# Performance work log

Hardware: AMD Instinct MI355X
Metric: run time of the kernel (lower is better)

The kernel has to match this reference:

```python
import jax, jax.numpy as jnp
import numpy as np

B, T, SZ, H = 16, 512, 512, 8
HD = SZ // H
D0, STD, GAMMA = 6.3, 1.4, 2.0
MAX_RPE = 16

def _dwconv(x, w):
    # depthwise conv1d, kernel 5, pad 2, groups=C, no bias; x: [B,T,C], w: [C,1,5]
    y = jax.lax.conv_general_dilated(x.transpose(0, 2, 1), w, (1,), [(2, 2)],
        dimension_numbers=('NCH', 'OIH', 'NCH'), feature_group_count=x.shape[-1])
    return y.transpose(0, 2, 1)

def _forward(mask, key, value, query, Wq, bq, Wk, bk, Wv, bv, Wcq, Wck, Wcv, Wgq, bgq, Wgk, bgk, Wgv, bgv, WmD, bmD, rpe_table, Wo, bo):
    q = query @ Wq.T + bq
    k = key @ Wk.T + bk
    v = value @ Wv.T + bv
    xn = key  # x_norm := key in the original forward
    # gated depthwise-conv context injection (qkv_context=[1,1,1], fuse='gate')
    qc = _dwconv(xn, Wcq)
    g = jax.nn.sigmoid(jnp.concatenate([q, qc], -1) @ Wgq.T + bgq)
    q = (1 - g) * q + g * qc
    kc = _dwconv(xn, Wck)
    g = jax.nn.sigmoid(jnp.concatenate([k, kc], -1) @ Wgk.T + bgk)
    k = (1 - g) * k + g * kc
    vc = _dwconv(xn, Wcv)
    g = jax.nn.sigmoid(jnp.concatenate([v, vc], -1) @ Wgv.T + bgv)
    v = (1 - g) * v + g * vc
    # learned Gaussian width: mod_D='head_share', mod_src='Q'
    off = (q @ WmD.T + bmD)[..., 0]                       # [B,T]
    m_D = D0 + 2.0 * STD * jnp.tanh(off / GAMMA)          # [B,T]
    qh = q.reshape(B, T, H, HD).transpose(0, 2, 1, 3) / jnp.sqrt(jnp.float32(HD))
    kh = k.reshape(B, T, H, HD).transpose(0, 2, 1, 3)
    vh = v.reshape(B, T, H, HD).transpose(0, 2, 1, 3)
    scores = jnp.einsum('bhqd,bhkd->bhqk', qh, kh)        # [B,H,T,T]
    idx = jnp.arange(T)
    d_int = idx[:, None] - idx[None, :]                   # i - j
    rd = jnp.clip(-d_int, -MAX_RPE, MAX_RPE) + MAX_RPE    # rpe indices [T,T]
    rpe = rpe_table[rd]                                   # [T,T,2*HD]
    rpe_k, rpe_v = rpe[..., :HD], rpe[..., HD:]
    scores = scores + jnp.einsum('bhqd,qkd->bhqk', qh, rpe_k)
    dist = d_int.astype(jnp.float32)
    scores = scores - dist ** 2 / (m_D[:, None, :, None] ** 2 / 2.0)
    scores = jnp.where(mask[:, None, :, :], -jnp.inf, scores)
    attn = jax.nn.softmax(scores, axis=-1)                # dropout is identity at eval
    ctx = jnp.einsum('bhqk,bhkd->bhqd', attn, vh) + jnp.einsum('bhqk,qkd->bhqd', attn, rpe_v)
    out = ctx.transpose(0, 2, 1, 3).reshape(B, T, SZ) @ Wo.T + bo
    return out

def setup_inputs():
    rng = jax.random.key(0)
    ks = jax.random.split(rng, 20)
    s = 0.02
    lin = lambda k, o, i: jax.random.normal(k, (o, i), jnp.float32) * s
    lengths = jax.random.randint(ks[3], (B,), T // 2, T + 1)
    mask = (jnp.arange(T)[None, :] >= lengths[:, None])[:, None, :]  # [B,1,T], True = pad
    return {
        'key': jax.random.normal(ks[0], (B, T, SZ), jnp.float32),
        'value': jax.random.normal(ks[1], (B, T, SZ), jnp.float32),
        'query': jax.random.normal(ks[2], (B, T, SZ), jnp.float32),
        'mask': mask,
        'Wq': lin(ks[4], SZ, SZ), 'bq': jnp.zeros((SZ,), jnp.float32),
        'Wk': lin(ks[5], SZ, SZ), 'bk': jnp.zeros((SZ,), jnp.float32),
        'Wv': lin(ks[6], SZ, SZ), 'bv': jnp.zeros((SZ,), jnp.float32),
        'Wcq': jax.random.normal(ks[7], (SZ, 1, 5), jnp.float32) * s,
        'Wck': jax.random.normal(ks[8], (SZ, 1, 5), jnp.float32) * s,
        'Wcv': jax.random.normal(ks[9], (SZ, 1, 5), jnp.float32) * s,
        'Wgq': lin(ks[10], 1, 2 * SZ), 'bgq': jnp.zeros((1,), jnp.float32),
        'Wgk': lin(ks[11], 1, 2 * SZ), 'bgk': jnp.zeros((1,), jnp.float32),
        'Wgv': lin(ks[12], 1, 2 * SZ), 'bgv': jnp.zeros((1,), jnp.float32),
        'WmD': lin(ks[13], 1, SZ), 'bmD': jnp.zeros((1,), jnp.float32),
        'rpe_table': jax.random.normal(ks[14], (2 * MAX_RPE + 1, 2 * HD), jnp.float32) * s,
        'Wo': lin(ks[15], SZ, SZ), 'bo': jnp.zeros((SZ,), jnp.float32),
    }

def reference(key, value, query, mask, Wq, bq, Wk, bk, Wv, bv, Wcq, Wck, Wcv, Wgq, bgq, Wgk, bgk, Wgv, bgv, WmD, bmD, rpe_table, Wo, bo):
    return _forward(mask, key, value, query, Wq, bq, Wk, bk, Wv, bv, Wcq, Wck, Wcv, Wgq, bgq, Wgk, bgk, Wgv, bgv, WmD, bmD, rpe_table, Wo, bo)
```

## Files before the change

### kernel.cpp

```cpp
#include <hip/hip_runtime.h>
#include <math.h>

#define NB 16
#define NT 512
#define NSZ 512
#define NH 8
#define NHD 64
#define MAXR 16

#define C_D0 6.3f
#define C_STD 1.4f
#define C_GAMMA 2.0f

#define NEGINF (-1e30f)
#define LOG2E 1.4426950408889634f
#define C1F   0.18033688011112042f

typedef unsigned short u16;
typedef __attribute__((ext_vector_type(8))) short bf16x8;
typedef __attribute__((ext_vector_type(4))) float f32x4;
typedef __attribute__((ext_vector_type(8))) unsigned short u16x8;
typedef __attribute__((ext_vector_type(4))) unsigned short u16x4;

__device__ __forceinline__ u16 f2b(float f) {
    union { float f; unsigned int u; } c; c.f = f;
    unsigned int u = c.u + 0x7FFFu + ((c.u >> 16) & 1u);
    return (u16)(u >> 16);
}
__device__ __forceinline__ float b2f(u16 h) {
    union { unsigned int u; float f; } c; c.u = ((unsigned int)h) << 16;
    return c.f;
}

#if __has_builtin(__builtin_amdgcn_exp2f)
__device__ __forceinline__ float exp2_fast(float x) { return __builtin_amdgcn_exp2f(x); }
#else
__device__ __forceinline__ float exp2_fast(float x) { return exp2f(x); }
#endif

#define GL2LDS(gp, lp) __builtin_amdgcn_global_load_lds( \
    (const __attribute__((address_space(1))) void*)(gp), \
    (__attribute__((address_space(3))) void*)(lp), 16, 0, 0)

#define SWU(r, c) ((((r) * 8) + ((c) ^ ((r) & 7))) * 8)
#define SWU16(r, c) ((((r) * 16) + ((c) ^ ((r) & 7))) * 8)

__global__ __launch_bounds__(256) void cvt4_bf16(
    const float* __restrict__ s0, const float* __restrict__ s1,
    const float* __restrict__ s2, const float* __restrict__ s3,
    u16* __restrict__ d0, u16* __restrict__ d1,
    u16* __restrict__ d2, u16* __restrict__ d3, int n)
{
    const float* s; u16* d;
    switch (blockIdx.y) {
        case 0: s = s0; d = d0; break;
        case 1: s = s1; d = d1; break;
        case 2: s = s2; d = d2; break;
        default: s = s3; d = d3; break;
    }
    int i = (blockIdx.x * 256 + threadIdx.x) * 8;
    if (i >= n) return;
    float4 a = *(const float4*)&s[i];
    float4 b = *(const float4*)&s[i + 4];
    u16x8 v;
    v[0]=f2b(a.x); v[1]=f2b(a.y); v[2]=f2b(a.z); v[3]=f2b(a.w);
    v[4]=f2b(b.x); v[5]=f2b(b.y); v[6]=f2b(b.z); v[7]=f2b(b.w);
    *(u16x8*)&d[i] = v;
}

__global__ __launch_bounds__(256) void wprep(
    const float* __restrict__ Wcq, const float* __restrict__ Wck,
    const float* __restrict__ Wcv, float* __restrict__ WcT)
{
    const int z = blockIdx.y;
    const float* src = z == 0 ? Wcq : (z == 1 ? Wck : Wcv);
    int idx = blockIdx.x * 256 + threadIdx.x;
    if (idx >= 2560) return;
    int c = idx / 5, j = idx % 5;
    WcT[(size_t)z * 2560 + j * 512 + c] = src[idx];
}

__global__ __launch_bounds__(256) void gemm_qkv(
    const float* __restrict__ A0, const float* __restrict__ A1, const float* __restrict__ A2,
    const u16* __restrict__ Wc,
    const float* __restrict__ bq, const float* __restrict__ bk, const float* __restrict__ bv,
    u16* __restrict__ pkv)
{
    __shared__ u16 Al[2][64 * 32];
    __shared__ u16 Bl[2][256 * 32];
    const int z = blockIdx.z;
    const float* A = z == 0 ? A0 : (z == 1 ? A1 : A2);
    const u16* W = Wc + (size_t)z * NSZ * NSZ;
    const float* bias = z == 0 ? bq : (z == 1 ? bk : bv);
    const int tid = threadIdx.x;
    const int m0 = blockIdx.x * 64;
    const int n0 = blockIdx.y * 256;
    const int w = tid >> 6, lane = tid & 63;
    const int wm = (w >> 1) * 32, wn = (w & 1) * 128;
    const int fr = lane & 15, fk = lane >> 4;

    const int arow = tid >> 2, acb = tid & 3;

    f32x4 acc[2][8] = {};

    {
        const float* ga = &A[(size_t)(m0 + arow) * NSZ + acb * 8];
        float4 a0 = *(const float4*)ga, a1 = *(const float4*)(ga + 4);
        #pragma unroll
        for (int p = 0; p < 4; ++p) {
            int s = tid + p * 256;
            int row = s >> 2, cb = s & 3;
            GL2LDS(&W[(size_t)(n0 + row) * NSZ + cb * 8], &Bl[0][s * 8]);
        }
        u16x8 v;
        v[0]=f2b(a0.x); v[1]=f2b(a0.y); v[2]=f2b(a0.z); v[3]=f2b(a0.w);
        v[4]=f2b(a1.x); v[5]=f2b(a1.y); v[6]=f2b(a1.z); v[7]=f2b(a1.w);
        *(u16x8*)&Al[0][tid * 8] = v;
    }
    __syncthreads();

    for (int t = 0; t < 16; ++t) {
        const int cur = t & 1, nxt = cur ^ 1;
        float4 a0n, a1n;
        const bool pre = (t < 15);
        if (pre) {
            const int k0 = (t + 1) * 32;
            const float* ga = &A[(size_t)(m0 + arow) * NSZ + k0 + acb * 8];
            a0n = *(const float4*)ga;
            a1n = *(const float4*)(ga + 4);
            #pragma unroll
            for (int p = 0; p < 4; ++p) {
                int s = tid + p * 256;
                int row = s >> 2, cb = s & 3;
                GL2LDS(&W[(size_t)(n0 + row) * NSZ + k0 + cb * 8], &Bl[nxt][s * 8]);
            }
        }
        bf16x8 af[2], bfr[8];
        #pragma unroll
        for (int mf = 0; mf < 2; ++mf)
            af[mf] = *(const bf16x8*)&Al[cur][(wm + mf * 16 + fr) * 32 + fk * 8];
        #pragma unroll
        for (int nf = 0; nf < 8; ++nf)
            bfr[nf] = *(const bf16x8*)&Bl[cur][(wn + nf * 16 + fr) * 32 + fk * 8];
        #pragma unroll
        for (int mf = 0; mf < 2; ++mf)
            #pragma unroll
            for (int nf = 0; nf < 8; ++nf)
                acc[mf][nf] = __builtin_amdgcn_mfma_f32_16x16x32_bf16(
                    af[mf], bfr[nf], acc[mf][nf], 0, 0, 0);
        if (pre) {
            u16x8 v;
            v[0]=f2b(a0n.x); v[1]=f2b(a0n.y); v[2]=f2b(a0n.z); v[3]=f2b(a0n.w);
            v[4]=f2b(a1n.x); v[5]=f2b(a1n.y); v[6]=f2b(a1n.z); v[7]=f2b(a1n.w);
            *(u16x8*)&Al[nxt][tid * 8] = v;
        }
        __syncthreads();
    }
    #pragma unroll
    for (int mf = 0; mf < 2; ++mf) {
        #pragma unroll
        for (int nf = 0; nf < 8; ++nf) {
            int col = n0 + wn + nf * 16 + fr;
            float bvv = bias[col];
            #pragma unroll
            for (int r = 0; r < 4; ++r) {
                int rowg = m0 + wm + mf * 16 + fk * 4 + r;
                pkv[(size_t)rowg * 1536 + z * 512 + col] = f2b(acc[mf][nf][r] + bvv);
            }
        }
    }
}

__global__ __launch_bounds__(256) void gemm_out(
    const u16* __restrict__ A, const u16* __restrict__ W,
    const float* __restrict__ bias, float* __restrict__ Cout, int M, int N, int K)
{
    __shared__ u16 Al[2][64 * 32];
    __shared__ u16 Bl[2][128 * 32];
    const int tid = threadIdx.x;
    const int m0 = blockIdx.x * 64;
    const int n0 = blockIdx.y * 128;
    const int w = tid >> 6, lane = tid & 63;
    const int wm = (w >> 1) * 32, wn = (w & 1) * 64;
    const int fr = lane & 15, fk = lane >> 4;

    f32x4 acc[2][4] = {};

    {
        int row = tid >> 2, cb = tid & 3;
        GL2LDS(&A[(size_t)(m0 + row) * K + cb * 8], &Al[0][tid * 8]);
        #pragma unroll
        for (int p = 0; p < 2; ++p) {
            int s = tid + p * 256;
            int r2 = s >> 2, c2 = s & 3;
            GL2LDS(&W[(size_t)(n0 + r2) * K + c2 * 8], &Bl[0][s * 8]);
        }
    }
    __syncthreads();

    const int nsteps = K / 32;
    for (int t = 0; t < nsteps; ++t) {
        const int cur = t & 1, nxt = cur ^ 1;
        if (t + 1 < nsteps) {
            const int k0 = (t + 1) * 32;
            int row = tid >> 2, cb = tid & 3;
            GL2LDS(&A[(size_t)(m0 + row) * K + k0 + cb * 8], &Al[nxt][tid * 8]);
            #pragma unroll
            for (int p = 0; p < 2; ++p) {
                int s = tid + p * 256;
                int r2 = s >> 2, c2 = s & 3;
                GL2LDS(&W[(size_t)(n0 + r2) * K + k0 + c2 * 8], &Bl[nxt][s * 8]);
            }
        }
        bf16x8 af[2], bfr[4];
        #pragma unroll
        for (int mf = 0; mf < 2; ++mf)
            af[mf] = *(const bf16x8*)&Al[cur][(wm + mf * 16 + fr) * 32 + fk * 8];
        #pragma unroll
        for (int nf = 0; nf < 4; ++nf)
            bfr[nf] = *(const bf16x8*)&Bl[cur][(wn + nf * 16 + fr) * 32 + fk * 8];
        #pragma unroll
        for (int mf = 0; mf < 2; ++mf)
            #pragma unroll
            for (int nf = 0; nf < 4; ++nf)
                acc[mf][nf] = __builtin_amdgcn_mfma_f32_16x16x32_bf16(
                    af[mf], bfr[nf], acc[mf][nf], 0, 0, 0);
        __syncthreads();
    }
    #pragma unroll
    for (int mf = 0; mf < 2; ++mf) {
        #pragma unroll
        for (int nf = 0; nf < 4; ++nf) {
            int col = n0 + wn + nf * 16 + fr;
            float bv = bias[col];
            #pragma unroll
            for (int r = 0; r < 4; ++r) {
                int rowg = m0 + wm + mf * 16 + fk * 4 + r;
                Cout[(size_t)rowg * N + col] = acc[mf][nf][r] + bv;
            }
        }
    }
}

__global__ void conv_gate_all(
    const float* __restrict__ xn, u16* __restrict__ pkv,
    u16* __restrict__ vpT,
    const float* __restrict__ WcT,
    const float* __restrict__ Wgq, const float* __restrict__ bgq,
    const float* __restrict__ Wgk, const float* __restrict__ bgk,
    const float* __restrict__ Wgv, const float* __restrict__ bgv,
    const float* __restrict__ WmD, const float* __restrict__ bmD,
    float* __restrict__ mD)
{
    __shared__ u16 lt[4][512];
    const int w = threadIdx.x >> 6, lane = threadIdx.x & 63;
    const int bt = blockIdx.x * 4 + w;
    const int b = bt >> 9, tpos = bt & (NT - 1);
    const int c0 = lane * 8;

    float x[5][8];
    #pragma unroll
    for (int j = 0; j < 5; ++j) {
        int tt = tpos + j - 2;
        if (tt >= 0 && tt < NT) {
            const float4* xp = (const float4*)&xn[((size_t)(b*NT + tt))*NSZ + c0];
            float4 u0 = xp[0], u1 = xp[1];
            x[j][0]=u0.x; x[j][1]=u0.y; x[j][2]=u0.z; x[j][3]=u0.w;
            x[j][4]=u1.x; x[j][5]=u1.y; x[j][6]=u1.z; x[j][7]=u1.w;
        } else {
            #pragma unroll
            for (int i = 0; i < 8; ++i) x[j][i] = 0.f;
        }
    }
    float aq[8] = {}, ak[8] = {}, av[8] = {};
    #pragma unroll
    for (int j = 0; j < 5; ++j) {
        const float* wq = &WcT[j * 512 + c0];
        const float* wk = &WcT[2560 + j * 512 + c0];
        const float* wv = &WcT[5120 + j * 512 + c0];
        float4 q0 = *(const float4*)wq, q1 = *(const float4*)(wq + 4);
        float4 k0 = *(const float4*)wk, k1 = *(const float4*)(wk + 4);
        float4 v0 = *(const float4*)wv, v1 = *(const float4*)(wv + 4);
        float wq8[8] = {q0.x,q0.y,q0.z,q0.w,q1.x,q1.y,q1.z,q1.w};
        float wk8[8] = {k0.x,k0.y,k0.z,k0.w,k1.x,k1.y,k1.z,k1.w};
        float wv8[8] = {v0.x,v0.y,v0.z,v0.w,v1.x,v1.y,v1.z,v1.w};
        #pragma unroll
        for (int i = 0; i < 8; ++i) {
            aq[i] += x[j][i] * wq8[i];
            ak[i] += x[j][i] * wk8[i];
            av[i] += x[j][i] * wv8[i];
        }
    }
    const size_t rb = (size_t)bt * 1536;
    u16x8 q8 = *(const u16x8*)&pkv[rb + c0];
    u16x8 k8 = *(const u16x8*)&pkv[rb + 512 + c0];
    u16x8 v8 = *(const u16x8*)&pkv[rb + 1024 + c0];

    float gql[8], gqh[8], gkl[8], gkh[8], gvl[8], gvh[8];
    {
        float4 a0 = *(const float4*)&Wgq[c0],      a1 = *(const float4*)&Wgq[c0 + 4];
        float4 a2 = *(const float4*)&Wgq[512 + c0], a3 = *(const float4*)&Wgq[512 + c0 + 4];
        gql[0]=a0.x;gql[1]=a0.y;gql[2]=a0.z;gql[3]=a0.w;gql[4]=a1.x;gql[5]=a1.y;gql[6]=a1.z;gql[7]=a1.w;
        gqh[0]=a2.x;gqh[1]=a2.y;gqh[2]=a2.z;gqh[3]=a2.w;gqh[4]=a3.x;gqh[5]=a3.y;gqh[6]=a3.z;gqh[7]=a3.w;
        float4 b0 = *(const float4*)&Wgk[c0],      b1 = *(const float4*)&Wgk[c0 + 4];
        float4 b2 = *(const float4*)&Wgk[512 + c0], b3 = *(const float4*)&Wgk[512 + c0 + 4];
        gkl[0]=b0.x;gkl[1]=b0.y;gkl[2]=b0.z;gkl[3]=b0.w;gkl[4]=b1.x;gkl[5]=b1.y;gkl[6]=b1.z;gkl[7]=b1.w;
        gkh[0]=b2.x;gkh[1]=b2.y;gkh[2]=b2.z;gkh[3]=b2.w;gkh[4]=b3.x;gkh[5]=b3.y;gkh[6]=b3.z;gkh[7]=b3.w;
        float4 c0v = *(const float4*)&Wgv[c0],      c1v = *(const float4*)&Wgv[c0 + 4];
        float4 c2v = *(const float4*)&Wgv[512 + c0], c3v = *(const float4*)&Wgv[512 + c0 + 4];
        gvl[0]=c0v.x;gvl[1]=c0v.y;gvl[2]=c0v.z;gvl[3]=c0v.w;gvl[4]=c1v.x;gvl[5]=c1v.y;gvl[6]=c1v.z;gvl[7]=c1v.w;
        gvh[0]=c2v.x;gvh[1]=c2v.y;gvh[2]=c2v.z;gvh[3]=c2v.w;gvh[4]=c3v.x;gvh[5]=c3v.y;gvh[6]=c3v.z;gvh[7]=c3v.w;
    }
    float sq = 0.f, sk = 0.f, sv = 0.f;
    #pragma unroll
    for (int i = 0; i < 8; ++i) {
        sq += b2f(q8[i]) * gql[i] + aq[i] * gqh[i];
        sk += b2f(k8[i]) * gkl[i] + ak[i] * gkh[i];
        sv += b2f(v8[i]) * gvl[i] + av[i] * gvh[i];
    }
    #pragma unroll
    for (int o = 1; o < 64; o <<= 1) {
        sq += __shfl_xor(sq, o, 64);
        sk += __shfl_xor(sk, o, 64);
        sv += __shfl_xor(sv, o, 64);
    }
    float gq = 1.f / (1.f + expf(-(sq + bgq[0])));
    float gk = 1.f / (1.f + expf(-(sk + bgk[0])));
    float gv = 1.f / (1.f + expf(-(sv + bgv[0])));

    float wm8[8];
    {
        float4 m0 = *(const float4*)&WmD[c0], m1 = *(const float4*)&WmD[c0 + 4];
        wm8[0]=m0.x;wm8[1]=m0.y;wm8[2]=m0.z;wm8[3]=m0.w;wm8[4]=m1.x;wm8[5]=m1.y;wm8[6]=m1.z;wm8[7]=m1.w;
    }
    u16x8 oq8, ok8, ov8;
    float smd = 0.f;
    #pragma unroll
    for (int i = 0; i < 8; ++i) {
        float oq = (1.f - gq) * b2f(q8[i]) + gq * aq[i];
        oq8[i] = f2b(oq);
        ok8[i] = f2b((1.f - gk) * b2f(k8[i]) + gk * ak[i]);
        ov8[i] = f2b((1.f - gv) * b2f(v8[i]) + gv * av[i]);
        smd += oq * wm8[i];
    }
    *(u16x8*)&pkv[rb + c0]       = oq8;
    *(u16x8*)&pkv[rb + 512 + c0] = ok8;
    *(u16x8*)&lt[w][c0] = ov8;
    #pragma unroll
    for (int o = 1; o < 64; o <<= 1) smd += __shfl_xor(smd, o, 64);
    if (lane == 0)
        mD[bt] = C_D0 + 2.f * C_STD * tanhf((smd + bmD[0]) / C_GAMMA);

    __syncthreads();
    const int t0g = (blockIdx.x * 4) & (NT - 1);
    const int b0g = (blockIdx.x * 4) >> 9;
    #pragma unroll
    for (int p2 = 0; p2 < 2; ++p2) {
        int c = threadIdx.x + p2 * 256;
        u16x4 o4;
        o4[0] = lt[0][c]; o4[1] = lt[1][c]; o4[2] = lt[2][c]; o4[3] = lt[3][c];
        *(u16x4*)&vpT[((size_t)(b0g * 512 + c)) * NT + t0g] = o4;
    }
}

__global__ __launch_bounds__(256) void attn_mfma(
    const u16* __restrict__ pkv, const u16* __restrict__ vpT,
    const float* __restrict__ mD, const int* __restrict__ mask,
    const float* __restrict__ rpe, u16* __restrict__ cxh)
{
    __shared__ __align__(16) char smem[70400];
    u16*  Ql    = (u16*)(smem);
    u16*  Kl    = (u16*)(smem + 8192);
    u16*  Vl    = (u16*)(smem + 24576);
    u16*  Pl    = (u16*)(smem + 40960);
    u16*  rpk   = (u16*)(smem + 40960);
    u16*  wA16  = (u16*)(smem + 57344);
    u16*  qdrl  = (u16*)(smem + 65536);
    float* inv2s= (float*)(smem + 70144);

    const int tid  = threadIdx.x;
// ... 116 lines not shown
                float qr = b2f(qdrl[lq * 36 + rd]);
                float fd = (float)(qg - kg);
                v = (s_[nf][r] + qr) * C1F - fd * fd * iv;
            }
            sc[nf] = v;
            mx = fmaxf(mx, v);
        }
        mx = fmaxf(mx, __shfl_xor(mx, 1, 64));
        mx = fmaxf(mx, __shfl_xor(mx, 2, 64));
        mx = fmaxf(mx, __shfl_xor(mx, 4, 64));
        mx = fmaxf(mx, __shfl_xor(mx, 8, 64));
        float rsum = 0.f, ls = 0.f, rs = 0.f;
        #pragma unroll
        for (int nf = 0; nf < 8; ++nf) {
            const int kg = w0 + nf * 16 + fr;
            float pv = exp2_fast(sc[nf] - mx);
            s_[nf][r] = pv;
            rsum += pv;
            int d = kg - qg;
            if (d <= -MAXR) ls += pv;
            else if (d >= MAXR) rs += pv;
            else {
                int bkt = d + MAXR;
                wA16[(lq * 8 + ((bkt >> 3) ^ (lq & 7))) * 8 + (bkt & 7)] = f2b(pv);
            }
        }
        rsum += __shfl_xor(rsum, 1, 64); rsum += __shfl_xor(rsum, 2, 64);
        rsum += __shfl_xor(rsum, 4, 64); rsum += __shfl_xor(rsum, 8, 64);
        ls += __shfl_xor(ls, 1, 64); ls += __shfl_xor(ls, 2, 64);
        ls += __shfl_xor(ls, 4, 64); ls += __shfl_xor(ls, 8, 64);
        rs += __shfl_xor(rs, 1, 64); rs += __shfl_xor(rs, 2, 64);
        rs += __shfl_xor(rs, 4, 64); rs += __shfl_xor(rs, 8, 64);
        li[r] = rsum;
        if (fr == 0) {
            wA16[(lq * 8 + (0 ^ (lq & 7))) * 8 + 0] = f2b(ls);
            wA16[(lq * 8 + (4 ^ (lq & 7))) * 8 + 0] = f2b(rs);
        }
    }

    #pragma unroll
    for (int r = 0; r < 4; ++r) {
        int lq = wq0 + fq * 4 + r;
        #pragma unroll
        for (int nf = 0; nf < 8; ++nf) {
            int k = nf * 16 + fr;
            int cc = k >> 3;
            Pl[(lq * 16 + (cc ^ (lq & 7))) * 8 + (k & 7)] = f2b(s_[nf][r]);
        }
    }

    f32x4 O[4] = {};
    #pragma unroll
    for (int ks = 0; ks < 4; ++ks) {
        bf16x8 ap = *(const bf16x8*)(Pl + ((wq0 + fr) * 16 + ((ks * 4 + fq) ^ (fr & 7))) * 8);
        #pragma unroll
        for (int nf = 0; nf < 4; ++nf) {
            bf16x8 vf = *(const bf16x8*)(Vl + ((nf * 16 + fr) * 16 + ((ks * 4 + fq) ^ (fr & 7))) * 8);
            O[nf] = __builtin_amdgcn_mfma_f32_16x16x32_bf16(ap, vf, O[nf], 0, 0, 0);
        }
    }
    __syncthreads();

    #pragma unroll
    for (int p = 0; p < 2; ++p) {
        int s = tid + p * 256;
        int d = s >> 3, cs = s & 7;
        u16x8 vv;
        #pragma unroll
        for (int j = 0; j < 8; ++j) {
            int rd = cs * 8 + j;
            vv[j] = (rd < 33) ? f2b(rpe[rd * 128 + 64 + d]) : (u16)0;
        }
        *(u16x8*)(Vl + SWU(d, cs)) = vv;
    }
    __syncthreads();

    {
        bf16x8 aw0 = *(const bf16x8*)(wA16 + SWU(wq0 + fr, fq));
        bf16x8 aw1 = *(const bf16x8*)(wA16 + SWU(wq0 + fr, 4 + fq));
        #pragma unroll
        for (int nf = 0; nf < 4; ++nf) {
            bf16x8 b0 = *(const bf16x8*)(Vl + SWU(nf * 16 + fr, fq));
            bf16x8 b1 = *(const bf16x8*)(Vl + SWU(nf * 16 + fr, 4 + fq));
            O[nf] = __builtin_amdgcn_mfma_f32_16x16x32_bf16(aw0, b0, O[nf], 0, 0, 0);
            O[nf] = __builtin_amdgcn_mfma_f32_16x16x32_bf16(aw1, b1, O[nf], 0, 0, 0);
        }
    }
    float invl[4];
    #pragma unroll
    for (int r = 0; r < 4; ++r) invl[r] = 1.f / li[r];
    #pragma unroll
    for (int r = 0; r < 4; ++r) {
        int lq = wq0 + fq * 4 + r;
        #pragma unroll
        for (int nf = 0; nf < 4; ++nf)
            Pl[lq * 64 + nf * 16 + fr] = f2b(O[nf][r] * invl[r]);
    }
    __syncthreads();
    #pragma unroll
    for (int j = 0; j < 2; ++j) {
        int s = w * 128 + j * 64 + lane;
        int rr = s >> 3, c8 = s & 7;
        u16x8 vv = *(const u16x8*)(Pl + rr * 64 + c8 * 8);
        *(u16x8*)&cxh[((size_t)(b*NT + q0 + rr)) * 512 + h * NHD + c8 * 8] = vv;
    }
}

extern "C" void kernel_launch(void* const* d_in, const int* in_sizes, int n_in,
                              void* d_out, int out_size, void* d_ws, size_t ws_size,
                              hipStream_t stream) {
    const float* key   = (const float*)d_in[0];
    const float* value = (const float*)d_in[1];
    const float* query = (const float*)d_in[2];
    const int*   mask  = (const int*)d_in[3];
    const float* Wq  = (const float*)d_in[4];
    const float* bq  = (const float*)d_in[5];
    const float* Wk  = (const float*)d_in[6];
    const float* bk  = (const float*)d_in[7];
    const float* Wv  = (const float*)d_in[8];
    const float* bv  = (const float*)d_in[9];
    const float* Wcq = (const float*)d_in[10];
    const float* Wck = (const float*)d_in[11];
    const float* Wcv = (const float*)d_in[12];
    const float* Wgq = (const float*)d_in[13];
    const float* bgq = (const float*)d_in[14];
    const float* Wgk = (const float*)d_in[15];
    const float* bgk = (const float*)d_in[16];
    const float* Wgv = (const float*)d_in[17];
    const float* bgv = (const float*)d_in[18];
    const float* WmD = (const float*)d_in[19];
    const float* bmD = (const float*)d_in[20];
    const float* rpe = (const float*)d_in[21];
    const float* Wo  = (const float*)d_in[22];
    const float* bo  = (const float*)d_in[23];
    float* out = (float*)d_out;

    const size_t NTOK = (size_t)NB * NT;
    const size_t NE   = NTOK * NSZ;
    const size_t NW   = (size_t)NSZ * NSZ;

    u16* ws16 = (u16*)d_ws;
    u16* pkv  = ws16;
    u16* wcat = pkv + NTOK * 1536;
    u16* woh  = wcat + 3 * NW;
    u16* vpT  = woh + NW;
    u16* cxh  = vpT + NE;
    float* mDb = (float*)(cxh + NE);
    float* WcT = mDb + NTOK;

    cvt4_bf16<<<dim3((unsigned)(NW/8/256), 4), 256, 0, stream>>>(
        Wq, Wk, Wv, Wo, wcat, wcat + NW, wcat + 2*NW, woh, (int)NW);
    wprep<<<dim3(10, 3), 256, 0, stream>>>(Wcq, Wck, Wcv, WcT);

    gemm_qkv<<<dim3(128, 2, 3), 256, 0, stream>>>(
        query, key, value, wcat, bq, bk, bv, pkv);

    conv_gate_all<<<(int)(NTOK / 4), 256, 0, stream>>>(
        key, pkv, vpT, WcT, Wgq, bgq, Wgk, bgk, Wgv, bgv, WmD, bmD, mDb);

    attn_mfma<<<dim3(128, 8), 256, 0, stream>>>(pkv, vpT, mDb, mask, rpe, cxh);

    gemm_out<<<dim3(128, 4), 256, 0, stream>>>(cxh, woh, bo, out, (int)NTOK, NSZ, NSZ);
}
```

Before: 108.6 us.

## Deepen GEMM pipelines to three LDS stages and shrink QKV tile width

The QKV projection GEMM now uses 64x128 tiles instead of 64x256, doubling the grid. It triple-buffers weight tiles in LDS, keeps two register-staged activation tiles in flight, and replaces __syncthreads with explicit waitcnt plus s_barrier. The output GEMM gets a three-stage LDS ring with vmcnt-based waits so global-to-LDS loads run two steps ahead. The goal is to hide global load latency behind MFMA work and improve occupancy, at the cost of more LDS per block and fragile hand-coded wait counts.

```diff
diff --git a/kernel.cpp b/kernel.cpp
--- a/kernel.cpp
+++ b/kernel.cpp
@@ -87,79 +87,135 @@
     u16* __restrict__ pkv)
 {
     __shared__ u16 Al[2][64 * 32];
-    __shared__ u16 Bl[2][256 * 32];
+    __shared__ u16 Wl[3][128 * 32];
     const int z = blockIdx.z;
     const float* A = z == 0 ? A0 : (z == 1 ? A1 : A2);
     const u16* W = Wc + (size_t)z * NSZ * NSZ;
     const float* bias = z == 0 ? bq : (z == 1 ? bk : bv);
     const int tid = threadIdx.x;
     const int m0 = blockIdx.x * 64;
-    const int n0 = blockIdx.y * 256;
+    const int n0 = blockIdx.y * 128;
     const int w = tid >> 6, lane = tid & 63;
-    const int wm = (w >> 1) * 32, wn = (w & 1) * 128;
+    const int wm = (w >> 1) * 32, wn = (w & 1) * 64;
     const int fr = lane & 15, fk = lane >> 4;
 
     const int arow = tid >> 2, acb = tid & 3;
-
-    f32x4 acc[2][8] = {};
-
+    const float* gA = &A[(size_t)(m0 + arow) * NSZ + acb * 8];
+    const int wrow = tid >> 2, wcb = tid & 3;
+
+    f32x4 acc[2][4] = {};
+
+    float4 t0a = *(const float4*)(gA);
+    float4 t0b = *(const float4*)(gA + 4);
+    #pragma unroll
+    for (int p = 0; p < 2; ++p) {
+        int s = tid + p * 256;
+        int row = s >> 2, cb = s & 3;
+        GL2LDS(&W[(size_t)(n0 + row) * NSZ + cb * 8], &Wl[0][s * 8]);
+    }
+    #pragma unroll
+    for (int p = 0; p < 2; ++p) {
+        int s = tid + p * 256;
+        int row = s >> 2, cb = s & 3;
+        GL2LDS(&W[(size_t)(n0 + row) * NSZ + 32 + cb * 8], &Wl[1][s * 8]);
+    }
+    float4 a0 = *(const float4*)(gA + 32);
+    float4 a1 = *(const float4*)(gA + 36);
     {
-        const float* ga = &A[(size_t)(m0 + arow) * NSZ + acb * 8];
-        float4 a0 = *(const float4*)ga, a1 = *(const float4*)(ga + 4);
-        #pragma unroll
-        for (int p = 0; p < 4; ++p) {
-            int s = tid + p * 256;
-            int row = s >> 2, cb = s & 3;
-            GL2LDS(&W[(size_t)(n0 + row) * NSZ + cb * 8], &Bl[0][s * 8]);
-        }
         u16x8 v;
-        v[0]=f2b(a0.x); v[1]=f2b(a0.y); v[2]=f2b(a0.z); v[3]=f2b(a0.w);
-        v[4]=f2b(a1.x); v[5]=f2b(a1.y); v[6]=f2b(a1.z); v[7]=f2b(a1.w);
+        v[0]=f2b(t0a.x); v[1]=f2b(t0a.y); v[2]=f2b(t0a.z); v[3]=f2b(t0a.w);
+        v[4]=f2b(t0b.x); v[5]=f2b(t0b.y); v[6]=f2b(t0b.z); v[7]=f2b(t0b.w);
         *(u16x8*)&Al[0][tid * 8] = v;
     }
-    __syncthreads();
-
-    for (int t = 0; t < 16; ++t) {
-        const int cur = t & 1, nxt = cur ^ 1;
-        float4 a0n, a1n;
-        const bool pre = (t < 15);
-        if (pre) {
-            const int k0 = (t + 1) * 32;
-            const float* ga = &A[(size_t)(m0 + arow) * NSZ + k0 + acb * 8];
-            a0n = *(const float4*)ga;
-            a1n = *(const float4*)(ga + 4);
-            #pragma unroll
-            for (int p = 0; p < 4; ++p) {
-                int s = tid + p * 256;
-                int row = s >> 2, cb = s & 3;
-                GL2LDS(&W[(size_t)(n0 + row) * NSZ + k0 + cb * 8], &Bl[nxt][s * 8]);
-            }
-        }
-        bf16x8 af[2], bfr[8];
-        #pragma unroll
-        for (int mf = 0; mf < 2; ++mf)
-            af[mf] = *(const bf16x8*)&Al[cur][(wm + mf * 16 + fr) * 32 + fk * 8];
-        #pragma unroll
-        for (int nf = 0; nf < 8; ++nf)
-            bfr[nf] = *(const bf16x8*)&Bl[cur][(wn + nf * 16 + fr) * 32 + fk * 8];
-        #pragma unroll
-        for (int mf = 0; mf < 2; ++mf)
-            #pragma unroll
-            for (int nf = 0; nf < 8; ++nf)
-                acc[mf][nf] = __builtin_amdgcn_mfma_f32_16x16x32_bf16(
-                    af[mf], bfr[nf], acc[mf][nf], 0, 0, 0);
-        if (pre) {
-            u16x8 v;
-            v[0]=f2b(a0n.x); v[1]=f2b(a0n.y); v[2]=f2b(a0n.z); v[3]=f2b(a0n.w);
-            v[4]=f2b(a1n.x); v[5]=f2b(a1n.y); v[6]=f2b(a1n.z); v[7]=f2b(a1n.w);
-            *(u16x8*)&Al[nxt][tid * 8] = v;
-        }
-        __syncthreads();
+    asm volatile("s_waitcnt lgkmcnt(0)" ::: "memory");
+    __builtin_amdgcn_sched_barrier(0);
+    __builtin_amdgcn_s_barrier();
+
+    float4 b0, b1;
+    int wiC = 0;
+    #pragma unroll 1
+    for (int tt = 0; tt < 8; ++tt) {
+        {
+            const int t = 2 * tt;
+            const int wiS = (wiC + 2 >= 3) ? wiC - 1 : wiC + 2;
+            bf16x8 af[2], bfr[4];
+            #pragma unroll
+            for (int mf = 0; mf < 2; ++mf)
+                af[mf] = *(const bf16x8*)&Al[t & 1][(wm + mf * 16 + fr) * 32 + fk * 8];
+            #pragma unroll
+            for (int nf = 0; nf < 4; ++nf)
+                bfr[nf] = *(const bf16x8*)&Wl[wiC][(wn + nf * 16 + fr) * 32 + fk * 8];
+            if (t < 14) {
+                const int k0 = (t + 2) * 32;
+                #pragma unroll
+                for (int p = 0; p < 2; ++p) {
+                    int s = tid + p * 256;
+                    int row = s >> 2, cb = s & 3;
+                    GL2LDS(&W[(size_t)(n0 + row) * NSZ + k0 + cb * 8], &Wl[wiS][s * 8]);
+                }
+                b0 = *(const float4*)(gA + k0);
+                b1 = *(const float4*)(gA + k0 + 4);
+            }
+            if (t < 15) {
+                u16x8 v;
+                v[0]=f2b(a0.x); v[1]=f2b(a0.y); v[2]=f2b(a0.z); v[3]=f2b(a0.w);
+                v[4]=f2b(a1.x); v[5]=f2b(a1.y); v[6]=f2b(a1.z); v[7]=f2b(a1.w);
+                *(u16x8*)&Al[(t + 1) & 1][tid * 8] = v;
+            }
+            #pragma unroll
+            for (int mf = 0; mf < 2; ++mf)
+                #pragma unroll
+                for (int nf = 0; nf < 4; ++nf)
+                    acc[mf][nf] = __builtin_amdgcn_mfma_f32_16x16x32_bf16(
+                        af[mf], bfr[nf], acc[mf][nf], 0, 0, 0);
+            asm volatile("s_waitcnt lgkmcnt(0)" ::: "memory");
+            __builtin_amdgcn_sched_barrier(0);
+            __builtin_amdgcn_s_barrier();
+            wiC = (wiC + 1 >= 3) ? 0 : wiC + 1;
+        }
+        {
+            const int t = 2 * tt + 1;
+            const int wiS = (wiC + 2 >= 3) ? wiC - 1 : wiC + 2;
+            bf16x8 af[2], bfr[4];
+            #pragma unroll
+            for (int mf = 0; mf < 2; ++mf)
+                af[mf] = *(const bf16x8*)&Al[t & 1][(wm + mf * 16 + fr) * 32 + fk * 8];
+            #pragma unroll
+            for (int nf = 0; nf < 4; ++nf)
+                bfr[nf] = *(const bf16x8*)&Wl[wiC][(wn + nf * 16 + fr) * 32 + fk * 8];
+            if (t < 14) {
+                const int k0 = (t + 2) * 32;
+                #pragma unroll
+                for (int p = 0; p < 2; ++p) {
+                    int s = tid + p * 256;
+                    int row = s >> 2, cb = s & 3;
+                    GL2LDS(&W[(size_t)(n0 + row) * NSZ + k0 + cb * 8], &Wl[wiS][s * 8]);
+                }
+                a0 = *(const float4*)(gA + k0);
+                a1 = *(const float4*)(gA + k0 + 4);
+            }
+            if (t < 15) {
+                u16x8 v;
+                v[0]=f2b(b0.x); v[1]=f2b(b0.y); v[2]=f2b(b0.z); v[3]=f2b(b0.w);
+                v[4]=f2b(b1.x); v[5]=f2b(b1.y); v[6]=f2b(b1.z); v[7]=f2b(b1.w);
+                *(u16x8*)&Al[(t + 1) & 1][tid * 8] = v;
+            }
+            #pragma unroll
+            for (int mf = 0; mf < 2; ++mf)
+                #pragma unroll
+                for (int nf = 0; nf < 4; ++nf)
+                    acc[mf][nf] = __builtin_amdgcn_mfma_f32_16x16x32_bf16(
+                        af[mf], bfr[nf], acc[mf][nf], 0, 0, 0);
+            asm volatile("s_waitcnt lgkmcnt(0)" ::: "memory");
+            __builtin_amdgcn_sched_barrier(0);
+            __builtin_amdgcn_s_barrier();
+            wiC = (wiC + 1 >= 3) ? 0 : wiC + 1;
+        }
     }
     #pragma unroll
     for (int mf = 0; mf < 2; ++mf) {
         #pragma unroll
-        for (int nf = 0; nf < 8; ++nf) {
+        for (int nf = 0; nf < 4; ++nf) {
             int col = n0 + wn + nf * 16 + fr;
             float bvv = bias[col];
             #pragma unroll
@@ -175,8 +231,8 @@
     const u16* __restrict__ A, const u16* __restrict__ W,
     const float* __restrict__ bias, float* __restrict__ Cout, int M, int N, int K)
 {
-    __shared__ u16 Al[2][64 * 32];
-    __shared__ u16 Bl[2][128 * 32];
+    __shared__ u16 Al[3][64 * 32];
+    __shared__ u16 Bl[3][128 * 32];
     const int tid = threadIdx.x;
     const int m0 = blockIdx.x * 64;
     const int n0 = blockIdx.y * 128;
@@ -186,46 +242,58 @@
 
     f32x4 acc[2][4] = {};
 
-    {
-        int row = tid >> 2, cb = tid & 3;
-        GL2LDS(&A[(size_t)(m0 + row) * K + cb * 8], &Al[0][tid * 8]);
+    #pragma unroll
+    for (int t0 = 0; t0 < 2; ++t0) {
+        int k0 = t0 * 32;
+        {
+            int row = tid >> 2, cb = tid & 3;
+            GL2LDS(&A[(size_t)(m0 + row) * K + k0 + cb * 8], &Al[t0][tid * 8]);
+        }
         #pragma unroll
         for (int p = 0; p < 2; ++p) {
             int s = tid + p * 256;
             int r2 = s >> 2, c2 = s & 3;
-            GL2LDS(&W[(size_t)(n0 + r2) * K + c2 * 8], &Bl[0][s * 8]);
-        }
-    }
-    __syncthreads();
-
-    const int nsteps = K / 32;
-    for (int t = 0; t < nsteps; ++t) {
-        const int cur = t & 1, nxt = cur ^ 1;
-        if (t + 1 < nsteps) {
-            const int k0 = (t + 1) * 32;
-            int row = tid >> 2, cb = tid & 3;
-            GL2LDS(&A[(size_t)(m0 + row) * K + k0 + cb * 8], &Al[nxt][tid * 8]);
+            GL2LDS(&W[(size_t)(n0 + r2) * K + k0 + c2 * 8], &Bl[t0][s * 8]);
+        }
+    }
+
+    int cur = 0;
+    #pragma unroll 1
+    for (int t = 0; t < 16; ++t) {
+        if (t < 15) asm volatile("s_waitcnt vmcnt(3)" ::: "memory");
+        else        asm volatile("s_waitcnt vmcnt(0)" ::: "memory");
+        __builtin_amdgcn_sched_barrier(0);
+        __builtin_amdgcn_s_barrier();
+
+        bf16x8 af[2], bfr[4];
+        #pragma unroll
+        for (int mf = 0; mf < 2; ++mf)
+            af[mf] = *(const bf16x8*)&Al[cur][(wm + mf * 16 + fr) * 32 + fk * 8];
+        #pragma unroll
+        for (int nf = 0; nf < 4; ++nf)
+            bfr[nf] = *(const bf16x8*)&Bl[cur][(wn + nf * 16 + fr) * 32 + fk * 8];
+
+        if (t < 14) {
+            const int k0 = (t + 2) * 32;
+            const int stg = (cur + 2 >= 3) ? cur - 1 : cur + 2;
+            {
+                int row = tid >> 2, cb = tid & 3;
+                GL2LDS(&A[(size_t)(m0 + row) * K + k0 + cb * 8], &Al[stg][tid * 8]);
+            }
             #pragma unroll
             for (int p = 0; p < 2; ++p) {
                 int s = tid + p * 256;
                 int r2 = s >> 2, c2 = s & 3;
-                GL2LDS(&W[(size_t)(n0 + r2) * K + k0 + c2 * 8], &Bl[nxt][s * 8]);
-            }
-        }
-        bf16x8 af[2], bfr[4];
-        #pragma unroll
-        for (int mf = 0; mf < 2; ++mf)
-            af[mf] = *(const bf16x8*)&Al[cur][(wm + mf * 16 + fr) * 32 + fk * 8];
-        #pragma unroll
-        for (int nf = 0; nf < 4; ++nf)
-            bfr[nf] = *(const bf16x8*)&Bl[cur][(wn + nf * 16 + fr) * 32 + fk * 8];
+                GL2LDS(&W[(size_t)(n0 + r2) * K + k0 + c2 * 8], &Bl[stg][s * 8]);
+            }
+        }
         #pragma unroll
         for (int mf = 0; mf < 2; ++mf)
             #pragma unroll
             for (int nf = 0; nf < 4; ++nf)
                 acc[mf][nf] = __builtin_amdgcn_mfma_f32_16x16x32_bf16(
                     af[mf], bfr[nf], acc[mf][nf], 0, 0, 0);
-        __syncthreads();
+        cur = (cur + 1 >= 3) ? 0 : cur + 1;
     }
     #pragma unroll
     for (int mf = 0; mf < 2; ++mf) {
@@ -648,7 +716,7 @@
         Wq, Wk, Wv, Wo, wcat, wcat + NW, wcat + 2*NW, woh, (int)NW);
     wprep<<<dim3(10, 3), 256, 0, stream>>>(Wcq, Wck, Wcv, WcT);
 
-    gemm_qkv<<<dim3(128, 2, 3), 256, 0, stream>>>(
+    gemm_qkv<<<dim3(128, 4, 3), 256, 0, stream>>>(
         query, key, value, wcat, bq, bk, bv, pkv);
 
     conv_gate_all<<<(int)(NTOK / 4), 256, 0, stream>>>(
```

Measured after the change: 108.1 us. Within noise of the previous version (-0.5%).

## Use BK=64 swizzled LDS tiles in QKV and output GEMMs, narrow QKV N-tile

Applied to the files above, without the earlier changes.

Both projection GEMMs now stage K-tiles of 64 instead of 32, halving the number of barrier-separated main-loop iterations, and store them in LDS with an XOR chunk swizzle meant to avoid bank conflicts on the fragment reads. The QKV GEMM also drops its N-tile from 256 to 128 and launches twice as many blocks, which lowers accumulator register pressure and raises occupancy and parallelism. In exchange, the A tile is loaded from global memory more times overall and each block uses more LDS per stage. This relies on a SWU swizzle helper that is assumed to be defined in the unseen part of the file.

```diff
diff --git a/kernel.cpp b/kernel.cpp
--- a/kernel.cpp
+++ b/kernel.cpp
@@ -86,80 +86,101 @@
     const float* __restrict__ bq, const float* __restrict__ bk, const float* __restrict__ bv,
     u16* __restrict__ pkv)
 {
-    __shared__ u16 Al[2][64 * 32];
-    __shared__ u16 Bl[2][256 * 32];
+    __shared__ u16 Al[2][64 * 64];
+    __shared__ u16 Wl[2][128 * 64];
     const int z = blockIdx.z;
     const float* A = z == 0 ? A0 : (z == 1 ? A1 : A2);
     const u16* W = Wc + (size_t)z * NSZ * NSZ;
     const float* bias = z == 0 ? bq : (z == 1 ? bk : bv);
     const int tid = threadIdx.x;
     const int m0 = blockIdx.x * 64;
-    const int n0 = blockIdx.y * 256;
+    const int n0 = blockIdx.y * 128;
     const int w = tid >> 6, lane = tid & 63;
-    const int wm = (w >> 1) * 32, wn = (w & 1) * 128;
+    const int wm = (w >> 1) * 32, wn = (w & 1) * 64;
     const int fr = lane & 15, fk = lane >> 4;
 
-    const int arow = tid >> 2, acb = tid & 3;
-
-    f32x4 acc[2][8] = {};
-
-    {
-        const float* ga = &A[(size_t)(m0 + arow) * NSZ + acb * 8];
-        float4 a0 = *(const float4*)ga, a1 = *(const float4*)(ga + 4);
-        #pragma unroll
-        for (int p = 0; p < 4; ++p) {
-            int s = tid + p * 256;
-            int row = s >> 2, cb = s & 3;
-            GL2LDS(&W[(size_t)(n0 + row) * NSZ + cb * 8], &Bl[0][s * 8]);
-        }
+    f32x4 acc[2][4] = {};
+
+    float4 na[2], nb[2];
+    #pragma unroll
+    for (int p = 0; p < 2; ++p) {
+        int s = tid + p * 256;
+        int row = s >> 3, ch = s & 7;
+        const float* ga = &A[(size_t)(m0 + row) * NSZ + ch * 8];
+        na[p] = *(const float4*)ga;
+        nb[p] = *(const float4*)(ga + 4);
+    }
+    #pragma unroll
+    for (int p = 0; p < 4; ++p) {
+        int s = tid + p * 256;
+        int row = s >> 3, ch = s & 7;
+        GL2LDS(&W[(size_t)(n0 + row) * NSZ + (ch ^ (row & 7)) * 8], &Wl[0][s * 8]);
+    }
+    #pragma unroll
+    for (int p = 0; p < 2; ++p) {
+        int s = tid + p * 256;
+        int row = s >> 3, ch = s & 7;
         u16x8 v;
-        v[0]=f2b(a0.x); v[1]=f2b(a0.y); v[2]=f2b(a0.z); v[3]=f2b(a0.w);
-        v[4]=f2b(a1.x); v[5]=f2b(a1.y); v[6]=f2b(a1.z); v[7]=f2b(a1.w);
-        *(u16x8*)&Al[0][tid * 8] = v;
-    }
-    __syncthreads();
-
-    for (int t = 0; t < 16; ++t) {
+        v[0]=f2b(na[p].x); v[1]=f2b(na[p].y); v[2]=f2b(na[p].z); v[3]=f2b(na[p].w);
+        v[4]=f2b(nb[p].x); v[5]=f2b(nb[p].y); v[6]=f2b(nb[p].z); v[7]=f2b(nb[p].w);
+        *(u16x8*)&Al[0][SWU(row, ch)] = v;
+    }
+    __syncthreads();
+
+    #pragma unroll 1
+    for (int t = 0; t < 8; ++t) {
         const int cur = t & 1, nxt = cur ^ 1;
-        float4 a0n, a1n;
-        const bool pre = (t < 15);
+        const bool pre = (t < 7);
         if (pre) {
-            const int k0 = (t + 1) * 32;
-            const float* ga = &A[(size_t)(m0 + arow) * NSZ + k0 + acb * 8];
-            a0n = *(const float4*)ga;
-            a1n = *(const float4*)(ga + 4);
+            const int k0 = (t + 1) * 64;
+            #pragma unroll
+            for (int p = 0; p < 2; ++p) {
+                int s = tid + p * 256;
+                int row = s >> 3, ch = s & 7;
+                const float* ga = &A[(size_t)(m0 + row) * NSZ + k0 + ch * 8];
+                na[p] = *(const float4*)ga;
+                nb[p] = *(const float4*)(ga + 4);
+            }
             #pragma unroll
             for (int p = 0; p < 4; ++p) {
                 int s = tid + p * 256;
-                int row = s >> 2, cb = s & 3;
-                GL2LDS(&W[(size_t)(n0 + row) * NSZ + k0 + cb * 8], &Bl[nxt][s * 8]);
-            }
-        }
-        bf16x8 af[2], bfr[8];
-        #pragma unroll
-        for (int mf = 0; mf < 2; ++mf)
-            af[mf] = *(const bf16x8*)&Al[cur][(wm + mf * 16 + fr) * 32 + fk * 8];
-        #pragma unroll
-        for (int nf = 0; nf < 8; ++nf)
-            bfr[nf] = *(const bf16x8*)&Bl[cur][(wn + nf * 16 + fr) * 32 + fk * 8];
-        #pragma unroll
-        for (int mf = 0; mf < 2; ++mf)
-            #pragma unroll
-            for (int nf = 0; nf < 8; ++nf)
-                acc[mf][nf] = __builtin_amdgcn_mfma_f32_16x16x32_bf16(
-                    af[mf], bfr[nf], acc[mf][nf], 0, 0, 0);
+                int row = s >> 3, ch = s & 7;
+                GL2LDS(&W[(size_t)(n0 + row) * NSZ + k0 + (ch ^ (row & 7)) * 8], &Wl[nxt][s * 8]);
+            }
+        }
+        #pragma unroll
+        for (int ks = 0; ks < 2; ++ks) {
+            bf16x8 af[2], bfr[4];
+            #pragma unroll
+            for (int mf = 0; mf < 2; ++mf)
+                af[mf] = *(const bf16x8*)&Al[cur][SWU(wm + mf * 16 + fr, ks * 4 + fk)];
+            #pragma unroll
+            for (int nf = 0; nf < 4; ++nf)
+                bfr[nf] = *(const bf16x8*)&Wl[cur][SWU(wn + nf * 16 + fr, ks * 4 + fk)];
+            #pragma unroll
+            for (int mf = 0; mf < 2; ++mf)
+                #pragma unroll
+                for (int nf = 0; nf < 4; ++nf)
+                    acc[mf][nf] = __builtin_amdgcn_mfma_f32_16x16x32_bf16(
+                        af[mf], bfr[nf], acc[mf][nf], 0, 0, 0);
+        }
         if (pre) {
-            u16x8 v;
-            v[0]=f2b(a0n.x); v[1]=f2b(a0n.y); v[2]=f2b(a0n.z); v[3]=f2b(a0n.w);
-            v[4]=f2b(a1n.x); v[5]=f2b(a1n.y); v[6]=f2b(a1n.z); v[7]=f2b(a1n.w);
-            *(u16x8*)&Al[nxt][tid * 8] = v;
+            #pragma unroll
+            for (int p = 0; p < 2; ++p) {
+                int s = tid + p * 256;
+                int row = s >> 3, ch = s & 7;
+                u16x8 v;
+                v[0]=f2b(na[p].x); v[1]=f2b(na[p].y); v[2]=f2b(na[p].z); v[3]=f2b(na[p].w);
+                v[4]=f2b(nb[p].x); v[5]=f2b(nb[p].y); v[6]=f2b(nb[p].z); v[7]=f2b(nb[p].w);
+                *(u16x8*)&Al[nxt][SWU(row, ch)] = v;
+            }
         }
         __syncthreads();
     }
     #pragma unroll
     for (int mf = 0; mf < 2; ++mf) {
         #pragma unroll
-        for (int nf = 0; nf < 8; ++nf) {
+        for (int nf = 0; nf < 4; ++nf) {
             int col = n0 + wn + nf * 16 + fr;
             float bvv = bias[col];
             #pragma unroll
@@ -175,8 +196,8 @@
     const u16* __restrict__ A, const u16* __restrict__ W,
     const float* __restrict__ bias, float* __restrict__ Cout, int M, int N, int K)
 {
-    __shared__ u16 Al[2][64 * 32];
-    __shared__ u16 Bl[2][128 * 32];
+    __shared__ u16 Al[2][64 * 64];
+    __shared__ u16 Bl[2][128 * 64];
     const int tid = threadIdx.x;
     const int m0 = blockIdx.x * 64;
     const int n0 = blockIdx.y * 128;
@@ -186,45 +207,54 @@
 
     f32x4 acc[2][4] = {};
 
-    {
-        int row = tid >> 2, cb = tid & 3;
-        GL2LDS(&A[(size_t)(m0 + row) * K + cb * 8], &Al[0][tid * 8]);
-        #pragma unroll
-        for (int p = 0; p < 2; ++p) {
-            int s = tid + p * 256;
-            int r2 = s >> 2, c2 = s & 3;
-            GL2LDS(&W[(size_t)(n0 + r2) * K + c2 * 8], &Bl[0][s * 8]);
-        }
-    }
-    __syncthreads();
-
-    const int nsteps = K / 32;
-    for (int t = 0; t < nsteps; ++t) {
+    #pragma unroll
+    for (int p = 0; p < 2; ++p) {
+        int s = tid + p * 256;
+        int row = s >> 3, ch = s & 7;
+        GL2LDS(&A[(size_t)(m0 + row) * K + (ch ^ (row & 7)) * 8], &Al[0][s * 8]);
+    }
+    #pragma unroll
+    for (int p = 0; p < 4; ++p) {
+        int s = tid + p * 256;
+        int row = s >> 3, ch = s & 7;
+        GL2LDS(&W[(size_t)(n0 + row) * K + (ch ^ (row & 7)) * 8], &Bl[0][s * 8]);
+    }
+    __syncthreads();
+
+    #pragma unroll 1
+    for (int t = 0; t < 8; ++t) {
         const int cur = t & 1, nxt = cur ^ 1;
-        if (t + 1 < nsteps) {
-            const int k0 = (t + 1) * 32;
-            int row = tid >> 2, cb = tid & 3;
-            GL2LDS(&A[(size_t)(m0 + row) * K + k0 + cb * 8], &Al[nxt][tid * 8]);
+        if (t < 7) {
+            const int k0 = (t + 1) * 64;
             #pragma unroll
             for (int p = 0; p < 2; ++p) {
                 int s = tid + p * 256;
-                int r2 = s >> 2, c2 = s & 3;
-                GL2LDS(&W[(size_t)(n0 + r2) * K + k0 + c2 * 8], &Bl[nxt][s * 8]);
-            }
-        }
-        bf16x8 af[2], bfr[4];
-        #pragma unroll
-        for (int mf = 0; mf < 2; ++mf)
-            af[mf] = *(const bf16x8*)&Al[cur][(wm + mf * 16 + fr) * 32 + fk * 8];
-        #pragma unroll
-        for (int nf = 0; nf < 4; ++nf)
-            bfr[nf] = *(const bf16x8*)&Bl[cur][(wn + nf * 16 + fr) * 32 + fk * 8];
-        #pragma unroll
-        for (int mf = 0; mf < 2; ++mf)
+                int row = s >> 3, ch = s & 7;
+                GL2LDS(&A[(size_t)(m0 + row) * K + k0 + (ch ^ (row & 7)) * 8], &Al[nxt][s * 8]);
+            }
+            #pragma unroll
+            for (int p = 0; p < 4; ++p) {
+                int s = tid + p * 256;
+                int row = s >> 3, ch = s & 7;
+                GL2LDS(&W[(size_t)(n0 + row) * K + k0 + (ch ^ (row & 7)) * 8], &Bl[nxt][s * 8]);
+            }
+        }
+        #pragma unroll
+        for (int ks = 0; ks < 2; ++ks) {
+            bf16x8 af[2], bfr[4];
+            #pragma unroll
+            for (int mf = 0; mf < 2; ++mf)
+                af[mf] = *(const bf16x8*)&Al[cur][SWU(wm + mf * 16 + fr, ks * 4 + fk)];
             #pragma unroll
             for (int nf = 0; nf < 4; ++nf)
-                acc[mf][nf] = __builtin_amdgcn_mfma_f32_16x16x32_bf16(
-                    af[mf], bfr[nf], acc[mf][nf], 0, 0, 0);
+                bfr[nf] = *(const bf16x8*)&Bl[cur][SWU(wn + nf * 16 + fr, ks * 4 + fk)];
+            #pragma unroll
+            for (int mf = 0; mf < 2; ++mf)
+                #pragma unroll
+                for (int nf = 0; nf < 4; ++nf)
+                    acc[mf][nf] = __builtin_amdgcn_mfma_f32_16x16x32_bf16(
+                        af[mf], bfr[nf], acc[mf][nf], 0, 0, 0);
+        }
         __syncthreads();
     }
     #pragma unroll
@@ -648,7 +678,7 @@
         Wq, Wk, Wv, Wo, wcat, wcat + NW, wcat + 2*NW, woh, (int)NW);
     wprep<<<dim3(10, 3), 256, 0, stream>>>(Wcq, Wck, Wcv, WcT);
 
-    gemm_qkv<<<dim3(128, 2, 3), 256, 0, stream>>>(
+    gemm_qkv<<<dim3(128, 4, 3), 256, 0, stream>>>(
         query, key, value, wcat, bq, bk, bv, pkv);
 
     conv_gate_all<<<(int)(NTOK / 4), 256, 0, stream>>>(
```

Result: no change. 107.6 us (-0.9%).

## Retile QKV and output GEMMs with swizzled LDS layouts

Applied to the files above, without the earlier changes.

The QKV projection GEMM drops from 64x256 to 64x64 output tiles, launching four times as many blocks for better CU occupancy, and both operands get XOR-swizzled LDS indexing to avoid bank conflicts. The output-projection GEMM moves to a 64-wide K step with a swizzled layout, halving the number of barrier iterations. The tradeoff is that smaller QKV tiles reload the fp32 A rows and convert them to bf16 eight times instead of twice, which raises global traffic and conversion work.

```diff
diff --git a/kernel.cpp b/kernel.cpp
--- a/kernel.cpp
+++ b/kernel.cpp
@@ -44,6 +44,8 @@
 
 #define SWU(r, c) ((((r) * 8) + ((c) ^ ((r) & 7))) * 8)
 #define SWU16(r, c) ((((r) * 16) + ((c) ^ ((r) & 7))) * 8)
+#define GSW(r)      (((r) >> 1) & 3)
+#define GIDX(r, c)  ((((r) * 4) + ((c) ^ GSW(r))) * 8)
 
 __global__ __launch_bounds__(256) void cvt4_bf16(
     const float* __restrict__ s0, const float* __restrict__ s1,
@@ -87,79 +89,72 @@
     u16* __restrict__ pkv)
 {
     __shared__ u16 Al[2][64 * 32];
-    __shared__ u16 Bl[2][256 * 32];
+    __shared__ u16 Wl[2][64 * 32];
     const int z = blockIdx.z;
     const float* A = z == 0 ? A0 : (z == 1 ? A1 : A2);
     const u16* W = Wc + (size_t)z * NSZ * NSZ;
     const float* bias = z == 0 ? bq : (z == 1 ? bk : bv);
     const int tid = threadIdx.x;
     const int m0 = blockIdx.x * 64;
-    const int n0 = blockIdx.y * 256;
+    const int n0 = blockIdx.y * 64;
     const int w = tid >> 6, lane = tid & 63;
-    const int wm = (w >> 1) * 32, wn = (w & 1) * 128;
+    const int wm = (w >> 1) * 32, wn = (w & 1) * 32;
     const int fr = lane & 15, fk = lane >> 4;
 
     const int arow = tid >> 2, acb = tid & 3;
-
-    f32x4 acc[2][8] = {};
+    const float* gA = &A[(size_t)(m0 + arow) * NSZ + acb * 8];
+    const int aldst = GIDX(arow, acb);
+
+    f32x4 acc[2][2] = {};
 
     {
-        const float* ga = &A[(size_t)(m0 + arow) * NSZ + acb * 8];
-        float4 a0 = *(const float4*)ga, a1 = *(const float4*)(ga + 4);
-        #pragma unroll
-        for (int p = 0; p < 4; ++p) {
-            int s = tid + p * 256;
-            int row = s >> 2, cb = s & 3;
-            GL2LDS(&W[(size_t)(n0 + row) * NSZ + cb * 8], &Bl[0][s * 8]);
-        }
+        float4 a0 = *(const float4*)gA, a1 = *(const float4*)(gA + 4);
+        int row = tid >> 2, cb = tid & 3;
+        GL2LDS(&W[(size_t)(n0 + row) * NSZ + (cb ^ GSW(row)) * 8], &Wl[0][tid * 8]);
         u16x8 v;
         v[0]=f2b(a0.x); v[1]=f2b(a0.y); v[2]=f2b(a0.z); v[3]=f2b(a0.w);
         v[4]=f2b(a1.x); v[5]=f2b(a1.y); v[6]=f2b(a1.z); v[7]=f2b(a1.w);
-        *(u16x8*)&Al[0][tid * 8] = v;
-    }
-    __syncthreads();
-
+        *(u16x8*)&Al[0][aldst] = v;
+    }
+    __syncthreads();
+
+    #pragma unroll 1
     for (int t = 0; t < 16; ++t) {
         const int cur = t & 1, nxt = cur ^ 1;
+        const bool pre = (t < 15);
         float4 a0n, a1n;
-        const bool pre = (t < 15);
         if (pre) {
             const int k0 = (t + 1) * 32;
-            const float* ga = &A[(size_t)(m0 + arow) * NSZ + k0 + acb * 8];
-            a0n = *(const float4*)ga;
-            a1n = *(const float4*)(ga + 4);
-            #pragma unroll
-            for (int p = 0; p < 4; ++p) {
-                int s = tid + p * 256;
-                int row = s >> 2, cb = s & 3;
-                GL2LDS(&W[(size_t)(n0 + row) * NSZ + k0 + cb * 8], &Bl[nxt][s * 8]);
-            }
-        }
-        bf16x8 af[2], bfr[8];
+            a0n = *(const float4*)(gA + k0);
+            a1n = *(const float4*)(gA + k0 + 4);
+            int row = tid >> 2, cb = tid & 3;
+            GL2LDS(&W[(size_t)(n0 + row) * NSZ + k0 + (cb ^ GSW(row)) * 8], &Wl[nxt][tid * 8]);
+        }
+        bf16x8 af[2], bfr[2];
         #pragma unroll
         for (int mf = 0; mf < 2; ++mf)
-            af[mf] = *(const bf16x8*)&Al[cur][(wm + mf * 16 + fr) * 32 + fk * 8];
-        #pragma unroll
-        for (int nf = 0; nf < 8; ++nf)
-            bfr[nf] = *(const bf16x8*)&Bl[cur][(wn + nf * 16 + fr) * 32 + fk * 8];
+            af[mf] = *(const bf16x8*)&Al[cur][GIDX(wm + mf * 16 + fr, fk)];
+        #pragma unroll
+        for (int nf = 0; nf < 2; ++nf)
+            bfr[nf] = *(const bf16x8*)&Wl[cur][GIDX(wn + nf * 16 + fr, fk)];
         #pragma unroll
         for (int mf = 0; mf < 2; ++mf)
             #pragma unroll
-            for (int nf = 0; nf < 8; ++nf)
+            for (int nf = 0; nf < 2; ++nf)
                 acc[mf][nf] = __builtin_amdgcn_mfma_f32_16x16x32_bf16(
                     af[mf], bfr[nf], acc[mf][nf], 0, 0, 0);
         if (pre) {
             u16x8 v;
             v[0]=f2b(a0n.x); v[1]=f2b(a0n.y); v[2]=f2b(a0n.z); v[3]=f2b(a0n.w);
             v[4]=f2b(a1n.x); v[5]=f2b(a1n.y); v[6]=f2b(a1n.z); v[7]=f2b(a1n.w);
-            *(u16x8*)&Al[nxt][tid * 8] = v;
+            *(u16x8*)&Al[nxt][aldst] = v;
         }
         __syncthreads();
     }
     #pragma unroll
     for (int mf = 0; mf < 2; ++mf) {
         #pragma unroll
-        for (int nf = 0; nf < 8; ++nf) {
+        for (int nf = 0; nf < 2; ++nf) {
             int col = n0 + wn + nf * 16 + fr;
             float bvv = bias[col];
             #pragma unroll
@@ -175,8 +170,8 @@
     const u16* __restrict__ A, const u16* __restrict__ W,
     const float* __restrict__ bias, float* __restrict__ Cout, int M, int N, int K)
 {
-    __shared__ u16 Al[2][64 * 32];
-    __shared__ u16 Bl[2][128 * 32];
+    __shared__ u16 Al[2][64 * 64];
+    __shared__ u16 Bl[2][128 * 64];
     const int tid = threadIdx.x;
     const int m0 = blockIdx.x * 64;
     const int n0 = blockIdx.y * 128;
@@ -186,45 +181,54 @@
 
     f32x4 acc[2][4] = {};
 
-    {
-        int row = tid >> 2, cb = tid & 3;
-        GL2LDS(&A[(size_t)(m0 + row) * K + cb * 8], &Al[0][tid * 8]);
-        #pragma unroll
-        for (int p = 0; p < 2; ++p) {
-            int s = tid + p * 256;
-            int r2 = s >> 2, c2 = s & 3;
-            GL2LDS(&W[(size_t)(n0 + r2) * K + c2 * 8], &Bl[0][s * 8]);
-        }
-    }
-    __syncthreads();
-
-    const int nsteps = K / 32;
-    for (int t = 0; t < nsteps; ++t) {
+    #pragma unroll
+    for (int p = 0; p < 2; ++p) {
+        int s = tid + p * 256;
+        int row = s >> 3, ch = s & 7;
+        GL2LDS(&A[(size_t)(m0 + row) * K + (ch ^ (row & 7)) * 8], &Al[0][s * 8]);
+    }
+    #pragma unroll
+    for (int p = 0; p < 4; ++p) {
+        int s = tid + p * 256;
+        int row = s >> 3, ch = s & 7;
+        GL2LDS(&W[(size_t)(n0 + row) * K + (ch ^ (row & 7)) * 8], &Bl[0][s * 8]);
+    }
+    __syncthreads();
+
+    #pragma unroll 1
+    for (int t = 0; t < 8; ++t) {
         const int cur = t & 1, nxt = cur ^ 1;
-        if (t + 1 < nsteps) {
-            const int k0 = (t + 1) * 32;
-            int row = tid >> 2, cb = tid & 3;
-            GL2LDS(&A[(size_t)(m0 + row) * K + k0 + cb * 8], &Al[nxt][tid * 8]);
+        if (t < 7) {
+            const int k0 = (t + 1) * 64;
             #pragma unroll
             for (int p = 0; p < 2; ++p) {
                 int s = tid + p * 256;
-                int r2 = s >> 2, c2 = s & 3;
-                GL2LDS(&W[(size_t)(n0 + r2) * K + k0 + c2 * 8], &Bl[nxt][s * 8]);
+                int row = s >> 3, ch = s & 7;
+                GL2LDS(&A[(size_t)(m0 + row) * K + k0 + (ch ^ (row & 7)) * 8], &Al[nxt][s * 8]);
             }
-        }
-        bf16x8 af[2], bfr[4];
-        #pragma unroll
-        for (int mf = 0; mf < 2; ++mf)
-            af[mf] = *(const bf16x8*)&Al[cur][(wm + mf * 16 + fr) * 32 + fk * 8];
-        #pragma unroll
-        for (int nf = 0; nf < 4; ++nf)
-            bfr[nf] = *(const bf16x8*)&Bl[cur][(wn + nf * 16 + fr) * 32 + fk * 8];
-        #pragma unroll
-        for (int mf = 0; mf < 2; ++mf)
+            #pragma unroll
+            for (int p = 0; p < 4; ++p) {
+                int s = tid + p * 256;
+                int row = s >> 3, ch = s & 7;
+                GL2LDS(&W[(size_t)(n0 + row) * K + k0 + (ch ^ (row & 7)) * 8], &Bl[nxt][s * 8]);
+            }
+        }
+        #pragma unroll
+        for (int ks = 0; ks < 2; ++ks) {
+            bf16x8 af[2], bfr[4];
+            #pragma unroll
+            for (int mf = 0; mf < 2; ++mf)
+                af[mf] = *(const bf16x8*)&Al[cur][SWU(wm + mf * 16 + fr, ks * 4 + fk)];
             #pragma unroll
             for (int nf = 0; nf < 4; ++nf)
-                acc[mf][nf] = __builtin_amdgcn_mfma_f32_16x16x32_bf16(
-                    af[mf], bfr[nf], acc[mf][nf], 0, 0, 0);
+                bfr[nf] = *(const bf16x8*)&Bl[cur][SWU(wn + nf * 16 + fr, ks * 4 + fk)];
+            #pragma unroll
+            for (int mf = 0; mf < 2; ++mf)
+                #pragma unroll
+                for (int nf = 0; nf < 4; ++nf)
+                    acc[mf][nf] = __builtin_amdgcn_mfma_f32_16x16x32_bf16(
+                        af[mf], bfr[nf], acc[mf][nf], 0, 0, 0);
+        }
         __syncthreads();
     }
     #pragma unroll
@@ -648,7 +652,7 @@
         Wq, Wk, Wv, Wo, wcat, wcat + NW, wcat + 2*NW, woh, (int)NW);
     wprep<<<dim3(10, 3), 256, 0, stream>>>(Wcq, Wck, Wcv, WcT);
 
-    gemm_qkv<<<dim3(128, 2, 3), 256, 0, stream>>>(
+    gemm_qkv<<<dim3(128, 8, 3), 256, 0, stream>>>(
         query, key, value, wcat, bq, bk, bv, pkv);
 
     conv_gate_all<<<(int)(NTOK / 4), 256, 0, stream>>>(
```

New measurement: 116.9 us. +7.6%, slower.
